# Performance work log

Measured on AMD Instinct MI355X. Metric: run time of the kernel, lower is better.

The kernel has to match this reference:

```python
import jax, jax.numpy as jnp
import numpy as np

T = 5
NORM_GROUPS = 16
EPS = 1e-5


def setup_inputs() -> dict:
    key = jax.random.key(0)
    weight = jax.random.normal(key, (2048, 18432), dtype=jnp.float32)
    return {"weight": weight}


def reference(weight):
    G = NORM_GROUPS
    out_ch = weight.shape[0]
    # [G, out_ch/G, fan_in]
    Z = weight.reshape(G, out_ch // G, -1)
    Zc = Z - Z.mean(axis=-1, keepdims=True)
    # Per-group covariance S: [G, n, n] with n = out_ch/G
    S = jnp.einsum('gik,gjk->gij', Zc, Zc)
    n = S.shape[-1]
    eye = jnp.eye(n, dtype=S.dtype)
    S = S + EPS * eye
    # Frobenius norm per group
    norm_S = jnp.sqrt(jnp.sum(S * S, axis=(1, 2), keepdims=True))
    S = S / norm_S
    # Newton-Schulz: B_{t+1} = 1.5*B_t - 0.5*B_t^3 @ S
    B = jnp.broadcast_to(eye, S.shape)
    for _ in range(T):  # T is a small fixed constant
        B3 = jnp.matmul(jnp.matmul(B, B), B)
        B = 1.5 * B - 0.5 * jnp.matmul(B3, S)
    W = jnp.matmul(B, Zc) / jnp.sqrt(norm_S)
    return W.reshape(weight.shape)
```

## Files before the change

kernel.cpp:

```cpp
#include <hip/hip_runtime.h>

#define G 16
#define N 128
#define FI 18432
#define SLABS 16
#define KS (FI / SLABS)
#define KT 32
#define NTILES (KS / KT)
#define EPSV 1e-5f

__global__ __launch_bounds__(256) void k_syrk(const float* __restrict__ Wt,
                                              float* __restrict__ partC,
                                              float* __restrict__ partRS) {
  const int slab = blockIdx.x, g = blockIdx.y;
  const int t = threadIdx.x;
  const int ty = t >> 4, tx = t & 15;
  __shared__ float As[KT][132];
  const float* base = Wt + (size_t)g * N * FI + (size_t)slab * KS;

  float acc[8][8];
#pragma unroll
  for (int i = 0; i < 8; ++i)
#pragma unroll
    for (int j = 0; j < 8; ++j) acc[i][j] = 0.f;
  float rs = 0.f;

  float4 stage[4];
#pragma unroll
  for (int j = 0; j < 4; ++j) {
    int f = j * 256 + t; int row = f >> 3, c4 = f & 7;
    stage[j] = *(const float4*)(base + (size_t)row * FI + c4 * 4);
  }

  for (int tile = 0; tile < NTILES; ++tile) {
    __syncthreads();
#pragma unroll
    for (int j = 0; j < 4; ++j) {
      int f = j * 256 + t; int row = f >> 3, c4 = f & 7;
      float4 v = stage[j];
      As[c4 * 4 + 0][row] = v.x; As[c4 * 4 + 1][row] = v.y;
      As[c4 * 4 + 2][row] = v.z; As[c4 * 4 + 3][row] = v.w;
    }
    __syncthreads();
    if (tile + 1 < NTILES) {
      const float* nb = base + (size_t)(tile + 1) * KT;
#pragma unroll
      for (int j = 0; j < 4; ++j) {
        int f = j * 256 + t; int row = f >> 3, c4 = f & 7;
        stage[j] = *(const float4*)(nb + (size_t)row * FI + c4 * 4);
      }
    }
    if (t < N) {
#pragma unroll
      for (int k = 0; k < KT; ++k) rs += As[k][t];
    }
    for (int k = 0; k < KT; ++k) {
      float4 a0 = *(const float4*)&As[k][ty * 8];
      float4 a1 = *(const float4*)&As[k][ty * 8 + 4];
      float4 b0 = *(const float4*)&As[k][tx * 4];
      float4 b1 = *(const float4*)&As[k][64 + tx * 4];
      float ar[8] = {a0.x, a0.y, a0.z, a0.w, a1.x, a1.y, a1.z, a1.w};
      float br[8] = {b0.x, b0.y, b0.z, b0.w, b1.x, b1.y, b1.z, b1.w};
#pragma unroll
      for (int i = 0; i < 8; ++i)
#pragma unroll
        for (int j = 0; j < 8; ++j) acc[i][j] += ar[i] * br[j];
    }
  }

  float* outp = partC + ((size_t)(g * SLABS + slab) << 14);
#pragma unroll
  for (int i = 0; i < 8; ++i) {
    int r = ty * 8 + i;
    *(float4*)(outp + r * N + tx * 4) =
        make_float4(acc[i][0], acc[i][1], acc[i][2], acc[i][3]);
    *(float4*)(outp + r * N + 64 + tx * 4) =
        make_float4(acc[i][4], acc[i][5], acc[i][6], acc[i][7]);
  }
  if (t < N) partRS[(g * SLABS + slab) * N + t] = rs;
}

__global__ __launch_bounds__(256) void k_reduce(const float* __restrict__ partC,
                                                const float* __restrict__ partRS,
                                                float* __restrict__ m_vec,
                                                float* __restrict__ S_un,
                                                float* __restrict__ normacc) {
  const int chunk = blockIdx.x;
  const int g = blockIdx.y;
  const int t = threadIdx.x;
  __shared__ float ms[N];
  if (t < N) {
    float s = 0.f;
    for (int sl = 0; sl < SLABS; ++sl) s += partRS[(g * SLABS + sl) * N + t];
    float mv = s * (1.f / (float)FI);
    ms[t] = mv;
    if (chunk == 0) m_vec[g * N + t] = mv;
  }
  __syncthreads();
  float ssq = 0.f;
#pragma unroll
  for (int i = 0; i < 8; ++i) {
    int e = chunk * 2048 + i * 256 + t;
    int row = e >> 7, col = e & 127;
    float v = 0.f;
    for (int sl = 0; sl < SLABS; ++sl)
      v += partC[((size_t)(g * SLABS + sl) << 14) + e];
    v -= (float)FI * ms[row] * ms[col];
    if (row == col) v += EPSV;
    S_un[((size_t)g << 14) + e] = v;
    ssq += v * v;
  }
  for (int off = 32; off; off >>= 1) ssq += __shfl_down(ssq, off, 64);
  __shared__ float red[4];
  if ((t & 63) == 0) red[t >> 6] = ssq;
  __syncthreads();
  if (t == 0) atomicAdd(normacc + g, red[0] + red[1] + red[2] + red[3]);
}

__global__ __launch_bounds__(256) void k_nsinit(const float* __restrict__ S_un,
                                                const float* __restrict__ normacc,
                                                float* __restrict__ S_n,
                                                float* __restrict__ Bm,
                                                float* __restrict__ scaleg) {
  const int chunk = blockIdx.x, g = blockIdx.y;
  const int t = threadIdx.x;
  float norm = sqrtf(normacc[g]);
  float inv = 1.f / norm;
  if (chunk == 0 && t == 0) scaleg[g] = 1.f / sqrtf(norm);
#pragma unroll
  for (int i = 0; i < 8; ++i) {
    int e = chunk * 2048 + i * 256 + t;
    int row = e >> 7, col = e & 127;
    float s = S_un[((size_t)g << 14) + e] * inv;
    S_n[((size_t)g << 14) + e] = s;
    Bm[((size_t)g << 14) + e] = (row == col ? 1.5f : 0.f) - 0.5f * s;
  }
}

__global__ __launch_bounds__(256) void k_nsmm2(const float* __restrict__ Bm,
                                               const float* __restrict__ S_n,
                                               float* __restrict__ T1,
                                               float* __restrict__ T2) {
  const int rb = blockIdx.x, which = blockIdx.y, g = blockIdx.z;
  const int t = threadIdx.x;
  const int r = t >> 4, c0 = (t & 15) * 4;
  const float* A = Bm + ((size_t)g << 14) + rb * 16 * N;
  const float* R = which ? (S_n + ((size_t)g << 14)) : (Bm + ((size_t)g << 14));
  float* outp = (which ? T2 : T1) + ((size_t)g << 14) + rb * 16 * N;
  __shared__ float Rs[N][132];
  __shared__ float As2[16][132];
#pragma unroll
  for (int j = 0; j < 16; ++j) {
    int f = j * 256 + t; int row = f >> 5, c4 = f & 31;
    *(float4*)&Rs[row][c4 * 4] = *(const float4*)(R + row * N + c4 * 4);
  }
#pragma unroll
  for (int j = 0; j < 2; ++j) {
    int f = j * 256 + t; int row = f >> 5, c4 = f & 31;
    *(float4*)&As2[row][c4 * 4] = *(const float4*)(A + row * N + c4 * 4);
  }
  __syncthreads();
  float acc[8];
#pragma unroll
  for (int j = 0; j < 8; ++j) acc[j] = 0.f;
  for (int k = 0; k < N; ++k) {
    float a = As2[r][k];
    float4 b0 = *(const float4*)&Rs[k][c0];
    float4 b1 = *(const float4*)&Rs[k][64 + c0];
    acc[0] += a * b0.x; acc[1] += a * b0.y; acc[2] += a * b0.z; acc[3] += a * b0.w;
    acc[4] += a * b1.x; acc[5] += a * b1.y; acc[6] += a * b1.z; acc[7] += a * b1.w;
  }
  *(float4*)(outp + r * N + c0) = make_float4(acc[0], acc[1], acc[2], acc[3]);
  *(float4*)(outp + r * N + 64 + c0) = make_float4(acc[4], acc[5], acc[6], acc[7]);
}

__global__ __launch_bounds__(256) void k_nsupd(const float* __restrict__ T1,
                                               const float* __restrict__ T2,
                                               float* __restrict__ Bm) {
  const int rb = blockIdx.x, g = blockIdx.y;
  const int t = threadIdx.x;
  const int r = t >> 4, c0 = (t & 15) * 4;
  const float* A = T1 + ((size_t)g << 14) + rb * 16 * N;
  const float* R = T2 + ((size_t)g << 14);
  float* Bp = Bm + ((size_t)g << 14) + rb * 16 * N;
  __shared__ float Rs[N][132];
  __shared__ float As2[16][132];
#pragma unroll
  for (int j = 0; j < 16; ++j) {
    int f = j * 256 + t; int row = f >> 5, c4 = f & 31;
    *(float4*)&Rs[row][c4 * 4] = *(const float4*)(R + row * N + c4 * 4);
  }
#pragma unroll
  for (int j = 0; j < 2; ++j) {
    int f = j * 256 + t; int row = f >> 5, c4 = f & 31;
    *(float4*)&As2[row][c4 * 4] = *(const float4*)(A + row * N + c4 * 4);
  }
  __syncthreads();
  float acc[8];
#pragma unroll
  for (int j = 0; j < 8; ++j) acc[j] = 0.f;
  for (int k = 0; k < N; ++k) {
    float a = As2[r][k];
    float4 b0 = *(const float4*)&Rs[k][c0];
    float4 b1 = *(const float4*)&Rs[k][64 + c0];
    acc[0] += a * b0.x; acc[1] += a * b0.y; acc[2] += a * b0.z; acc[3] += a * b0.w;
    acc[4] += a * b1.x; acc[5] += a * b1.y; acc[6] += a * b1.z; acc[7] += a * b1.w;
  }
  float4 bo0 = *(const float4*)(Bp + r * N + c0);
  float4 bo1 = *(const float4*)(Bp + r * N + 64 + c0);
  *(float4*)(Bp + r * N + c0) =
      make_float4(1.5f * bo0.x - 0.5f * acc[0], 1.5f * bo0.y - 0.5f * acc[1],
                  1.5f * bo0.z - 0.5f * acc[2], 1.5f * bo0.w - 0.5f * acc[3]);
  *(float4*)(Bp + r * N + 64 + c0) =
      make_float4(1.5f * bo1.x - 0.5f * acc[4], 1.5f * bo1.y - 0.5f * acc[5],
                  1.5f * bo1.z - 0.5f * acc[6], 1.5f * bo1.w - 0.5f * acc[7]);
}

#define CT 128
__global__ __launch_bounds__(256) void k_final(const float* __restrict__ Wt,
                                               const float* __restrict__ Bm,
                                               const float* __restrict__ m_vec,
                                               const float* __restrict__ scaleg,
                                               float* __restrict__ outp) {
  const int ct = blockIdx.x;
  const int rh = blockIdx.y;
  const int g = blockIdx.z;
  const int t = threadIdx.x;
  const int ty = t >> 4, tx = t & 15;
  __shared__ float Bs[64][132];
  __shared__ float Zs[KT][132];
  __shared__ float cs[64];
  __shared__ float msh[N];

  const float* Bbase = Bm + ((size_t)g << 14) + rh * 64 * N;
#pragma unroll
  for (int j = 0; j < 8; ++j) {
    int f = j * 256 + t; int row = f >> 5, c4 = f & 31;
    *(float4*)&Bs[row][c4 * 4] = *(const float4*)(Bbase + row * N + c4 * 4);
  }
  if (t < N) msh[t] = m_vec[g * N + t];
  __syncthreads();
  if (t < 64) {
    float c = 0.f;
    for (int k = 0; k < N; ++k) c += Bs[t][k] * msh[k];
    cs[t] = c;
  }

  float acc[4][8];
#pragma unroll
  for (int i = 0; i < 4; ++i)
#pragma unroll
    for (int j = 0; j < 8; ++j) acc[i][j] = 0.f;

  const float* zbase = Wt + (size_t)g * N * FI + (size_t)ct * CT;
  for (int kc = 0; kc < 4; ++kc) {
    __syncthreads();
#pragma unroll
    for (int j = 0; j < 4; ++j) {
      int f = j * 256 + t; int kr = f >> 5, c4 = f & 31;
      *(float4*)&Zs[kr][c4 * 4] =
          *(const float4*)(zbase + (size_t)(kc * KT + kr) * FI + c4 * 4);
    }
    __syncthreads();
#pragma unroll
    for (int kb = 0; kb < 8; ++kb) {
      float br[4][4];
#pragma unroll
      for (int i = 0; i < 4; ++i)
        *(float4*)br[i] = *(const float4*)&Bs[ty * 4 + i][kc * KT + kb * 4];
#pragma unroll
      for (int kk = 0; kk < 4; ++kk) {
        float4 z0 = *(const float4*)&Zs[kb * 4 + kk][tx * 4];
        float4 z1 = *(const float4*)&Zs[kb * 4 + kk][64 + tx * 4];
        float zr[8] = {z0.x, z0.y, z0.z, z0.w, z1.x, z1.y, z1.z, z1.w};
#pragma unroll
        for (int i = 0; i < 4; ++i)
#pragma unroll
          for (int j = 0; j < 8; ++j) acc[i][j] += br[i][kk] * zr[j];
      }
    }
  }

  const float scl = scaleg[g];
  size_t obase = ((size_t)(g * N + rh * 64)) * FI + (size_t)ct * CT;
#pragma unroll
  for (int i = 0; i < 4; ++i) {
    int r = ty * 4 + i;
    float cc = cs[r];
    *(float4*)(outp + obase + (size_t)r * FI + tx * 4) =
        make_float4((acc[i][0] - cc) * scl, (acc[i][1] - cc) * scl,
                    (acc[i][2] - cc) * scl, (acc[i][3] - cc) * scl);
    *(float4*)(outp + obase + (size_t)r * FI + 64 + tx * 4) =
        make_float4((acc[i][4] - cc) * scl, (acc[i][5] - cc) * scl,
                    (acc[i][6] - cc) * scl, (acc[i][7] - cc) * scl);
  }
}

extern "C" void kernel_launch(void* const* d_in, const int* in_sizes, int n_in,
                              void* d_out, int out_size, void* d_ws, size_t ws_size,
                              hipStream_t stream) {
  (void)in_sizes; (void)n_in; (void)out_size; (void)ws_size;
  const float* Wt = (const float*)d_in[0];
  float* outp = (float*)d_out;

  float* ws = (float*)d_ws;
  float* partC = ws;
  float* partRS = partC + 4194304;
  float* m_vec = partRS + 32768;
  float* S_un = m_vec + 2048;
  float* S_n = S_un + 262144;
  float* Bm = S_n + 262144;
  float* T1 = Bm + 262144;
  float* T2 = T1 + 262144;
  float* normacc = T2 + 262144;
  float* scaleg = normacc + 16;

  hipMemsetAsync(normacc, 0, G * sizeof(float), stream);
  k_syrk<<<dim3(SLABS, G), 256, 0, stream>>>(Wt, partC, partRS);
  k_reduce<<<dim3(8, G), 256, 0, stream>>>(partC, partRS, m_vec, S_un, normacc);
  k_nsinit<<<dim3(8, G), 256, 0, stream>>>(S_un, normacc, S_n, Bm, scaleg);
  for (int it = 0; it < 4; ++it) {
    k_nsmm2<<<dim3(8, 2, G), 256, 0, stream>>>(Bm, S_n, T1, T2);
    k_nsupd<<<dim3(8, G), 256, 0, stream>>>(T1, T2, Bm);
  }
  k_final<<<dim3(FI / CT, 2, G), 256, 0, stream>>>(Wt, Bm, m_vec, scaleg, outp);
}
```

Before: 510.2 us.

## Use split-bf16 MFMA for covariance and final projection matmuls

The SYRK covariance kernel and the final B·Zc projection move from scalar FP32 FMA loops to bf16 MFMA instructions. Each FP32 value is split into a high and a low bf16 part, and four MFMAs per tile recover close to FP32 accuracy. The SYRK slab count is raised to 32 when the workspace allows, which gives more blocks for parallelism, and the reduce grid is widened to match. The final kernel now handles all 128 rows per block and holds B in registers. The split adds conversion work and some rounding error compared with pure FP32. Both kernels were compute-heavy scalar FP32 GEMMs, so the aim is to cut their compute time.

```diff
diff --git a/kernel.cpp b/kernel.cpp
--- a/kernel.cpp
+++ b/kernel.cpp
@@ -3,83 +3,130 @@
 #define G 16
 #define N 128
 #define FI 18432
-#define SLABS 16
-#define KS (FI / SLABS)
-#define KT 32
-#define NTILES (KS / KT)
 #define EPSV 1e-5f
 
-__global__ __launch_bounds__(256) void k_syrk(const float* __restrict__ Wt,
-                                              float* __restrict__ partC,
-                                              float* __restrict__ partRS) {
+typedef __attribute__((ext_vector_type(8))) short short8;
+typedef __attribute__((ext_vector_type(4))) float f32x4;
+
+__device__ inline unsigned short bf16_rn(float x) {
+  unsigned u = __float_as_uint(x);
+  u += 0x7FFFu + ((u >> 16) & 1u);
+  return (unsigned short)(u >> 16);
+}
+__device__ inline float bf16f(unsigned short h) {
+  return __uint_as_float(((unsigned)h) << 16);
+}
+__device__ inline void split2(float x, unsigned short& h, unsigned short& l) {
+  h = bf16_rn(x);
+  l = bf16_rn(x - bf16f(h));
+}
+__device__ inline f32x4 zero4() {
+  f32x4 z = {0.f, 0.f, 0.f, 0.f};
+  return z;
+}
+
+template <int SLABS>
+__global__ __launch_bounds__(256, 2) void k_syrk(const float* __restrict__ Wt,
+                                                 float* __restrict__ partC,
+                                                 float* __restrict__ partRS) {
+  constexpr int KS = FI / SLABS;
+  constexpr int NCH = KS / 64;
   const int slab = blockIdx.x, g = blockIdx.y;
   const int t = threadIdx.x;
-  const int ty = t >> 4, tx = t & 15;
-  __shared__ float As[KT][132];
+  const int w = t >> 6, lane = t & 63;
+  __shared__ __align__(16) unsigned short Hs[128][72];
+  __shared__ __align__(16) unsigned short Ls[128][72];
+
   const float* base = Wt + (size_t)g * N * FI + (size_t)slab * KS;
 
-  float acc[8][8];
-#pragma unroll
-  for (int i = 0; i < 8; ++i)
-#pragma unroll
-    for (int j = 0; j < 8; ++j) acc[i][j] = 0.f;
-  float rs = 0.f;
-
-  float4 stage[4];
-#pragma unroll
-  for (int j = 0; j < 4; ++j) {
-    int f = j * 256 + t; int row = f >> 3, c4 = f & 7;
-    stage[j] = *(const float4*)(base + (size_t)row * FI + c4 * 4);
-  }
-
-  for (int tile = 0; tile < NTILES; ++tile) {
+  f32x4 acc[2][8];
+#pragma unroll
+  for (int i = 0; i < 2; ++i)
+#pragma unroll
+    for (int j = 0; j < 8; ++j) acc[i][j] = zero4();
+  float rs[8];
+#pragma unroll
+  for (int j = 0; j < 8; ++j) rs[j] = 0.f;
+
+  for (int ch = 0; ch < NCH; ++ch) {
+    float4 v[8];
+#pragma unroll
+    for (int j = 0; j < 8; ++j) {
+      int f = t + 256 * j;
+      int row = f >> 4, c4 = f & 15;
+      v[j] = *(const float4*)(base + (size_t)row * FI + ch * 64 + c4 * 4);
+    }
     __syncthreads();
 #pragma unroll
-    for (int j = 0; j < 4; ++j) {
-      int f = j * 256 + t; int row = f >> 3, c4 = f & 7;
-      float4 v = stage[j];
-      As[c4 * 4 + 0][row] = v.x; As[c4 * 4 + 1][row] = v.y;
-      As[c4 * 4 + 2][row] = v.z; As[c4 * 4 + 3][row] = v.w;
+    for (int j = 0; j < 8; ++j) {
+      int f = t + 256 * j;
+      int row = f >> 4, c4 = f & 15;
+      rs[j] += v[j].x + v[j].y + v[j].z + v[j].w;
+      unsigned short h0, h1, h2, h3, l0, l1, l2, l3;
+      split2(v[j].x, h0, l0);
+      split2(v[j].y, h1, l1);
+      split2(v[j].z, h2, l2);
+      split2(v[j].w, h3, l3);
+      *(uint2*)&Hs[row][c4 * 4] =
+          make_uint2((unsigned)h0 | ((unsigned)h1 << 16),
+                     (unsigned)h2 | ((unsigned)h3 << 16));
+      *(uint2*)&Ls[row][c4 * 4] =
+          make_uint2((unsigned)l0 | ((unsigned)l1 << 16),
+                     (unsigned)l2 | ((unsigned)l3 << 16));
     }
     __syncthreads();
-    if (tile + 1 < NTILES) {
-      const float* nb = base + (size_t)(tile + 1) * KT;
-#pragma unroll
-      for (int j = 0; j < 4; ++j) {
-        int f = j * 256 + t; int row = f >> 3, c4 = f & 7;
-        stage[j] = *(const float4*)(nb + (size_t)row * FI + c4 * 4);
-      }
-    }
-    if (t < N) {
-#pragma unroll
-      for (int k = 0; k < KT; ++k) rs += As[k][t];
-    }
-    for (int k = 0; k < KT; ++k) {
-      float4 a0 = *(const float4*)&As[k][ty * 8];
-      float4 a1 = *(const float4*)&As[k][ty * 8 + 4];
-      float4 b0 = *(const float4*)&As[k][tx * 4];
-      float4 b1 = *(const float4*)&As[k][64 + tx * 4];
-      float ar[8] = {a0.x, a0.y, a0.z, a0.w, a1.x, a1.y, a1.z, a1.w};
-      float br[8] = {b0.x, b0.y, b0.z, b0.w, b1.x, b1.y, b1.z, b1.w};
-#pragma unroll
-      for (int i = 0; i < 8; ++i)
-#pragma unroll
-        for (int j = 0; j < 8; ++j) acc[i][j] += ar[i] * br[j];
+#pragma unroll
+    for (int kk = 0; kk < 2; ++kk) {
+      const int kof = kk * 32 + (lane >> 4) * 8;
+      short8 ah[2], al[2];
+#pragma unroll
+      for (int i = 0; i < 2; ++i) {
+        int r = (2 * w + i) * 16 + (lane & 15);
+        ah[i] = *(const short8*)&Hs[r][kof];
+        al[i] = *(const short8*)&Ls[r][kof];
+      }
+#pragma unroll
+      for (int jb = 0; jb < 8; ++jb) {
+        int r = jb * 16 + (lane & 15);
+        short8 zh = *(const short8*)&Hs[r][kof];
+        short8 zl = *(const short8*)&Ls[r][kof];
+#pragma unroll
+        for (int i = 0; i < 2; ++i) {
+          acc[i][jb] = __builtin_amdgcn_mfma_f32_16x16x32_bf16(ah[i], zh, acc[i][jb], 0, 0, 0);
+          acc[i][jb] = __builtin_amdgcn_mfma_f32_16x16x32_bf16(ah[i], zl, acc[i][jb], 0, 0, 0);
+          acc[i][jb] = __builtin_amdgcn_mfma_f32_16x16x32_bf16(al[i], zh, acc[i][jb], 0, 0, 0);
+          acc[i][jb] = __builtin_amdgcn_mfma_f32_16x16x32_bf16(al[i], zl, acc[i][jb], 0, 0, 0);
+        }
+      }
     }
   }
 
   float* outp = partC + ((size_t)(g * SLABS + slab) << 14);
 #pragma unroll
-  for (int i = 0; i < 8; ++i) {
-    int r = ty * 8 + i;
-    *(float4*)(outp + r * N + tx * 4) =
-        make_float4(acc[i][0], acc[i][1], acc[i][2], acc[i][3]);
-    *(float4*)(outp + r * N + 64 + tx * 4) =
-        make_float4(acc[i][4], acc[i][5], acc[i][6], acc[i][7]);
-  }
-  if (t < N) partRS[(g * SLABS + slab) * N + t] = rs;
-}
-
+  for (int i = 0; i < 2; ++i)
+#pragma unroll
+    for (int jb = 0; jb < 8; ++jb)
+#pragma unroll
+      for (int r = 0; r < 4; ++r) {
+        int row = (2 * w + i) * 16 + (lane >> 4) * 4 + r;
+        int col = jb * 16 + (lane & 15);
+        outp[row * N + col] = acc[i][jb][r];
+      }
+#pragma unroll
+  for (int j = 0; j < 8; ++j) {
+    float s = rs[j];
+    s += __shfl_down(s, 8, 16);
+    s += __shfl_down(s, 4, 16);
+    s += __shfl_down(s, 2, 16);
+    s += __shfl_down(s, 1, 16);
+    if ((t & 15) == 0) {
+      int row = (t >> 4) + 16 * j;
+      partRS[(size_t)(g * SLABS + slab) * N + row] = s;
+    }
+  }
+}
+
+template <int SLABS>
 __global__ __launch_bounds__(256) void k_reduce(const float* __restrict__ partC,
                                                 const float* __restrict__ partRS,
                                                 float* __restrict__ m_vec,
@@ -91,7 +138,7 @@
   __shared__ float ms[N];
   if (t < N) {
     float s = 0.f;
-    for (int sl = 0; sl < SLABS; ++sl) s += partRS[(g * SLABS + sl) * N + t];
+    for (int sl = 0; sl < SLABS; ++sl) s += partRS[(size_t)(g * SLABS + sl) * N + t];
     float mv = s * (1.f / (float)FI);
     ms[t] = mv;
     if (chunk == 0) m_vec[g * N + t] = mv;
@@ -99,8 +146,8 @@
   __syncthreads();
   float ssq = 0.f;
 #pragma unroll
-  for (int i = 0; i < 8; ++i) {
-    int e = chunk * 2048 + i * 256 + t;
+  for (int i = 0; i < 4; ++i) {
+    int e = chunk * 1024 + i * 256 + t;
     int row = e >> 7, col = e & 127;
     float v = 0.f;
     for (int sl = 0; sl < SLABS; ++sl)
@@ -216,112 +263,148 @@
                   1.5f * bo1.z - 0.5f * acc[6], 1.5f * bo1.w - 0.5f * acc[7]);
 }
 
-#define CT 128
-__global__ __launch_bounds__(256) void k_final(const float* __restrict__ Wt,
-                                               const float* __restrict__ Bm,
-                                               const float* __restrict__ m_vec,
-                                               const float* __restrict__ scaleg,
-                                               float* __restrict__ outp) {
+__global__ __launch_bounds__(256, 2) void k_final(const float* __restrict__ Wt,
+                                                  const float* __restrict__ Bm,
+                                                  const float* __restrict__ m_vec,
+                                                  const float* __restrict__ scaleg,
+                                                  float* __restrict__ outp) {
   const int ct = blockIdx.x;
-  const int rh = blockIdx.y;
-  const int g = blockIdx.z;
-  const int t = threadIdx.x;
-  const int ty = t >> 4, tx = t & 15;
-  __shared__ float Bs[64][132];
-  __shared__ float Zs[KT][132];
-  __shared__ float cs[64];
+  const int g = blockIdx.y;
+  const int t = threadIdx.x;
+  const int w = t >> 6, lane = t & 63;
+  __shared__ __align__(16) unsigned short Zh[64][136];
+  __shared__ __align__(16) unsigned short Zl[64][136];
   __shared__ float msh[N];
 
-  const float* Bbase = Bm + ((size_t)g << 14) + rh * 64 * N;
-#pragma unroll
-  for (int j = 0; j < 8; ++j) {
-    int f = j * 256 + t; int row = f >> 5, c4 = f & 31;
-    *(float4*)&Bs[row][c4 * 4] = *(const float4*)(Bbase + row * N + c4 * 4);
-  }
   if (t < N) msh[t] = m_vec[g * N + t];
   __syncthreads();
-  if (t < 64) {
-    float c = 0.f;
-    for (int k = 0; k < N; ++k) c += Bs[t][k] * msh[k];
-    cs[t] = c;
-  }
-
-  float acc[4][8];
-#pragma unroll
-  for (int i = 0; i < 4; ++i)
-#pragma unroll
-    for (int j = 0; j < 8; ++j) acc[i][j] = 0.f;
-
-  const float* zbase = Wt + (size_t)g * N * FI + (size_t)ct * CT;
-  for (int kc = 0; kc < 4; ++kc) {
+
+  short8 bh[2][4], bl[2][4];
+  float cs[2] = {0.f, 0.f};
+  const float* Bg = Bm + ((size_t)g << 14);
+#pragma unroll
+  for (int i = 0; i < 2; ++i) {
+    int row = (2 * w + i) * 16 + (lane & 15);
+#pragma unroll
+    for (int kk = 0; kk < 4; ++kk) {
+      int kof = kk * 32 + (lane >> 4) * 8;
+      float4 p0 = *(const float4*)(Bg + row * N + kof);
+      float4 p1 = *(const float4*)(Bg + row * N + kof + 4);
+      unsigned short h[8], l[8];
+      split2(p0.x, h[0], l[0]); split2(p0.y, h[1], l[1]);
+      split2(p0.z, h[2], l[2]); split2(p0.w, h[3], l[3]);
+      split2(p1.x, h[4], l[4]); split2(p1.y, h[5], l[5]);
+      split2(p1.z, h[6], l[6]); split2(p1.w, h[7], l[7]);
+      bh[i][kk] = (short8){(short)h[0], (short)h[1], (short)h[2], (short)h[3],
+                           (short)h[4], (short)h[5], (short)h[6], (short)h[7]};
+      bl[i][kk] = (short8){(short)l[0], (short)l[1], (short)l[2], (short)l[3],
+                           (short)l[4], (short)l[5], (short)l[6], (short)l[7]};
+      cs[i] += p0.x * msh[kof] + p0.y * msh[kof + 1] + p0.z * msh[kof + 2] +
+               p0.w * msh[kof + 3] + p1.x * msh[kof + 4] + p1.y * msh[kof + 5] +
+               p1.z * msh[kof + 6] + p1.w * msh[kof + 7];
+    }
+    cs[i] += __shfl_xor(cs[i], 16);
+    cs[i] += __shfl_xor(cs[i], 32);
+  }
+  const float scl = scaleg[g];
+
+  for (int sc = 0; sc < 2; ++sc) {
+    const float* zb = Wt + (size_t)g * N * FI + ct * 128 + sc * 64;
     __syncthreads();
 #pragma unroll
-    for (int j = 0; j < 4; ++j) {
-      int f = j * 256 + t; int kr = f >> 5, c4 = f & 31;
-      *(float4*)&Zs[kr][c4 * 4] =
-          *(const float4*)(zbase + (size_t)(kc * KT + kr) * FI + c4 * 4);
+    for (int jj = 0; jj < 4; ++jj) {
+      int idx = t + 256 * jj;
+      int n4 = idx & 15, k2 = idx >> 4;
+      float4 a = *(const float4*)(zb + (size_t)(2 * k2) * FI + n4 * 4);
+      float4 b = *(const float4*)(zb + (size_t)(2 * k2 + 1) * FI + n4 * 4);
+      int k2s = k2 ^ ((n4 & 3) << 2);
+      float av[4] = {a.x, a.y, a.z, a.w};
+      float bv[4] = {b.x, b.y, b.z, b.w};
+#pragma unroll
+      for (int c = 0; c < 4; ++c) {
+        int col = n4 * 4 + c;
+        unsigned short h0, l0, h1, l1;
+        split2(av[c], h0, l0);
+        split2(bv[c], h1, l1);
+        *(unsigned*)&Zh[col][2 * k2s] = (unsigned)h0 | ((unsigned)h1 << 16);
+        *(unsigned*)&Zl[col][2 * k2s] = (unsigned)l0 | ((unsigned)l1 << 16);
+      }
     }
     __syncthreads();
-#pragma unroll
-    for (int kb = 0; kb < 8; ++kb) {
-      float br[4][4];
-#pragma unroll
-      for (int i = 0; i < 4; ++i)
-        *(float4*)br[i] = *(const float4*)&Bs[ty * 4 + i][kc * KT + kb * 4];
-#pragma unroll
-      for (int kk = 0; kk < 4; ++kk) {
-        float4 z0 = *(const float4*)&Zs[kb * 4 + kk][tx * 4];
-        float4 z1 = *(const float4*)&Zs[kb * 4 + kk][64 + tx * 4];
-        float zr[8] = {z0.x, z0.y, z0.z, z0.w, z1.x, z1.y, z1.z, z1.w};
-#pragma unroll
-        for (int i = 0; i < 4; ++i)
-#pragma unroll
-          for (int j = 0; j < 8; ++j) acc[i][j] += br[i][kk] * zr[j];
-      }
-    }
-  }
-
-  const float scl = scaleg[g];
-  size_t obase = ((size_t)(g * N + rh * 64)) * FI + (size_t)ct * CT;
-#pragma unroll
-  for (int i = 0; i < 4; ++i) {
-    int r = ty * 4 + i;
-    float cc = cs[r];
-    *(float4*)(outp + obase + (size_t)r * FI + tx * 4) =
-        make_float4((acc[i][0] - cc) * scl, (acc[i][1] - cc) * scl,
-                    (acc[i][2] - cc) * scl, (acc[i][3] - cc) * scl);
-    *(float4*)(outp + obase + (size_t)r * FI + 64 + tx * 4) =
-        make_float4((acc[i][4] - cc) * scl, (acc[i][5] - cc) * scl,
-                    (acc[i][6] - cc) * scl, (acc[i][7] - cc) * scl);
+    f32x4 acc[2][4];
+#pragma unroll
+    for (int i = 0; i < 2; ++i)
+#pragma unroll
+      for (int jb = 0; jb < 4; ++jb) acc[i][jb] = zero4();
+#pragma unroll
+    for (int kk = 0; kk < 4; ++kk) {
+#pragma unroll
+      for (int jb = 0; jb < 4; ++jb) {
+        int col = jb * 16 + (lane & 15);
+        int k2b = (kk * 16 + (lane >> 4) * 4) ^ (((col >> 2) & 3) << 2);
+        short8 zh8 = *(const short8*)&Zh[col][2 * k2b];
+        short8 zl8 = *(const short8*)&Zl[col][2 * k2b];
+#pragma unroll
+        for (int i = 0; i < 2; ++i) {
+          acc[i][jb] = __builtin_amdgcn_mfma_f32_16x16x32_bf16(bh[i][kk], zh8, acc[i][jb], 0, 0, 0);
+          acc[i][jb] = __builtin_amdgcn_mfma_f32_16x16x32_bf16(bh[i][kk], zl8, acc[i][jb], 0, 0, 0);
+          acc[i][jb] = __builtin_amdgcn_mfma_f32_16x16x32_bf16(bl[i][kk], zh8, acc[i][jb], 0, 0, 0);
+          acc[i][jb] = __builtin_amdgcn_mfma_f32_16x16x32_bf16(bl[i][kk], zl8, acc[i][jb], 0, 0, 0);
+        }
+      }
+    }
+#pragma unroll
+    for (int i = 0; i < 2; ++i)
+#pragma unroll
+      for (int r = 0; r < 4; ++r) {
+        int rloc = (lane >> 4) * 4 + r;
+        float csr = __shfl(cs[i], rloc, 64);
+        int row = (2 * w + i) * 16 + rloc;
+#pragma unroll
+        for (int jb = 0; jb < 4; ++jb) {
+          int col = ct * 128 + sc * 64 + jb * 16 + (lane & 15);
+          outp[(size_t)(g * N + row) * FI + col] = (acc[i][jb][r] - csr) * scl;
+        }
+      }
   }
 }
 
 extern "C" void kernel_launch(void* const* d_in, const int* in_sizes, int n_in,
                               void* d_out, int out_size, void* d_ws, size_t ws_size,
                               hipStream_t stream) {
-  (void)in_sizes; (void)n_in; (void)out_size; (void)ws_size;
+  (void)in_sizes; (void)n_in; (void)out_size;
   const float* Wt = (const float*)d_in[0];
   float* outp = (float*)d_out;
-
   float* ws = (float*)d_ws;
+
+  const size_t need32 =
+      ((size_t)32 * G * 16384 + (size_t)32 * G * N + G * N + 5 * 262144 + 64) * 4;
+  const bool big = ws_size >= need32;
+  const int slabs = big ? 32 : 16;
+
   float* partC = ws;
-  float* partRS = partC + 4194304;
-  float* m_vec = partRS + 32768;
-  float* S_un = m_vec + 2048;
+  float* partRS = partC + (size_t)slabs * G * 16384;
+  float* m_vec = partRS + (size_t)slabs * G * N;
+  float* S_un = m_vec + G * N;
   float* S_n = S_un + 262144;
   float* Bm = S_n + 262144;
   float* T1 = Bm + 262144;
   float* T2 = T1 + 262144;
   float* normacc = T2 + 262144;
-  float* scaleg = normacc + 16;
+  float* scaleg = normacc + G;
 
   hipMemsetAsync(normacc, 0, G * sizeof(float), stream);
-  k_syrk<<<dim3(SLABS, G), 256, 0, stream>>>(Wt, partC, partRS);
-  k_reduce<<<dim3(8, G), 256, 0, stream>>>(partC, partRS, m_vec, S_un, normacc);
+  if (big) {
+    k_syrk<32><<<dim3(32, G), 256, 0, stream>>>(Wt, partC, partRS);
+    k_reduce<32><<<dim3(16, G), 256, 0, stream>>>(partC, partRS, m_vec, S_un, normacc);
+  } else {
+    k_syrk<16><<<dim3(16, G), 256, 0, stream>>>(Wt, partC, partRS);
+    k_reduce<16><<<dim3(16, G), 256, 0, stream>>>(partC, partRS, m_vec, S_un, normacc);
+  }
   k_nsinit<<<dim3(8, G), 256, 0, stream>>>(S_un, normacc, S_n, Bm, scaleg);
   for (int it = 0; it < 4; ++it) {
     k_nsmm2<<<dim3(8, 2, G), 256, 0, stream>>>(Bm, S_n, T1, T2);
     k_nsupd<<<dim3(8, G), 256, 0, stream>>>(T1, T2, Bm);
   }
-  k_final<<<dim3(FI / CT, 2, G), 256, 0, stream>>>(Wt, Bm, m_vec, scaleg, outp);
-}
+  k_final<<<dim3(FI / 128, G), 256, 0, stream>>>(Wt, Bm, m_vec, scaleg, outp);
+}
```

New measurement: 426.2 us. -16.5%, faster.
